# Optimization experiments

Hardware: AMD Instinct MI355X
Metric: run time of the kernel (lower is better)

## Reference

```python
import jax, jax.numpy as jnp
import numpy as np

N_A, N_B, C, M, E = 40000, 80000, 256, 4, 250000
NUM_HEADS = 4


def setup_inputs() -> dict:
    key = jax.random.key(0)
    ks = jax.random.split(key, 32)
    p = lambda k, shp: jax.random.normal(k, shp, dtype=jnp.float32) * 0.02
    src_ab = jax.random.randint(ks[0], (M, 1, E), 0, N_A, dtype=jnp.int32)
    dst_ab = jax.random.randint(ks[1], (M, 1, E), 0, N_B, dtype=jnp.int32)
    src_ba = jax.random.randint(ks[2], (M, 1, E), 0, N_B, dtype=jnp.int32)
    dst_ba = jax.random.randint(ks[3], (M, 1, E), 0, N_A, dtype=jnp.int32)
    mp_w = jax.random.uniform(ks[4], (M,), dtype=jnp.float32) + 0.1
    mp_w = mp_w / mp_w.sum()  # normalized metapath_counts buffer
    return {
        "x_a": jax.random.normal(ks[5], (N_A, C), jnp.float32),
        "x_b": jax.random.normal(ks[6], (N_B, C), jnp.float32),
        "edges_ab": jnp.concatenate([src_ab, dst_ab], axis=1),  # [M,2,E]
        "edges_ba": jnp.concatenate([src_ba, dst_ba], axis=1),  # [M,2,E]
        "wl1": p(ks[7], (M, C, C)), "wr1": p(ks[8], (M, C, C)), "b1": p(ks[9], (M, C)),
        "wl2": p(ks[10], (M, C, C)), "wr2": p(ks[11], (M, C, C)), "b2": p(ks[12], (M, C)),
        "outw": p(ks[13], (M, C, C)), "outb": p(ks[14], (M, C)),
        "mp_weights": mp_w,
        "in_proj_w": p(ks[15], (3 * C, C)), "in_proj_b": p(ks[16], (3 * C,)),
        "attn_out_w": p(ks[17], (C, C)), "attn_out_b": p(ks[18], (C,)),
        "mlp1_w": p(ks[19], (C, C)), "mlp1_b": p(ks[20], (C,)),
        "mlp2_w": p(ks[21], (C, 1)), "mlp2_b": p(ks[22], (1,)),
    }


def _sage(x_src, x_dst, src, dst, n_dst, wl, wr, b):
    # SAGEConv (mean aggr): lin_l(mean_{src->dst} x_src) + lin_r(x_dst) + b
    msg = jax.ops.segment_sum(x_src[src], dst, num_segments=n_dst)
    cnt = jax.ops.segment_sum(jnp.ones(src.shape, x_src.dtype), dst, num_segments=n_dst)
    mean = msg / jnp.maximum(cnt, 1.0)[:, None]
    return mean @ wl + x_dst @ wr + b


def _forward(x_a, x_b, edges_ab, edges_ba, wl1, wr1, b1, wl2, wr2, b2, outw, outb,
             mp_weights, in_proj_w, in_proj_b, attn_out_w, attn_out_b,
             mlp1_w, mlp1_b, mlp2_w, mlp2_b):
    embs = []
    for m in range(M):  # small fixed set of metapath GNNs (structurally distinct params)
        h_b = jax.nn.relu(_sage(x_a, x_b, edges_ab[m, 0], edges_ab[m, 1], N_B,
                                wl1[m], wr1[m], b1[m]))
        h_a = jax.nn.relu(_sage(h_b, x_a, edges_ba[m, 0], edges_ba[m, 1], N_A,
                                wl2[m], wr2[m], b2[m]))
        embs.append(h_a @ outw[m] + outb[m])  # out_proj on start node type
    x = jnp.stack(embs, axis=1) * mp_weights[None, :, None]  # [N_A, M, C]
    # MultiheadAttention (batch_first, self-attention over metapath axis)
    qkv = x @ in_proj_w.T + in_proj_b
    q, k, v = jnp.split(qkv, 3, axis=-1)
    d = C // NUM_HEADS
    q = q.reshape(N_A, M, NUM_HEADS, d)
    k = k.reshape(N_A, M, NUM_HEADS, d)
    v = v.reshape(N_A, M, NUM_HEADS, d)
    scores = jnp.einsum('nqhd,nkhd->nhqk', q, k) / jnp.sqrt(jnp.float32(d))
    attn = jax.nn.softmax(scores, axis=-1)
    o = jnp.einsum('nhqk,nkhd->nqhd', attn, v).reshape(N_A, M, C)
    o = o @ attn_out_w.T + attn_out_b
    pooled = o.mean(axis=1)  # [N_A, C]
    h = jax.nn.relu(pooled @ mlp1_w + mlp1_b)
    return (h @ mlp2_w + mlp2_b).squeeze(-1)  # [N_A]


def reference(x_a, x_b, edges_ab, edges_ba, wl1, wr1, b1, wl2, wr2, b2, outw, outb,
              mp_weights, in_proj_w, in_proj_b, attn_out_w, attn_out_b,
              mlp1_w, mlp1_b, mlp2_w, mlp2_b):
    return _forward(x_a, x_b, edges_ab, edges_ba, wl1, wr1, b1, wl2, wr2, b2,
                    outw, outb, mp_weights, in_proj_w, in_proj_b,
                    attn_out_w, attn_out_b, mlp1_w, mlp1_b, mlp2_w, mlp2_b)
```

## Files before the change

kernel.cpp:

```cpp
#include <hip/hip_runtime.h>
#include <hip/hip_bf16.h>
#include <hip/hip_fp16.h>


#define N_A 40000
#define N_B 80000
#define CDIM 256
#define MP 4
#define EDG 250000

using f16x8 = __attribute__((ext_vector_type(8))) _Float16;
using f32x4 = __attribute__((ext_vector_type(4))) float;

__device__ __forceinline__ float ldf(const float* p) { return *p; }
__device__ __forceinline__ float ldf(const __half* p) { return __half2float(*p); }
__device__ __forceinline__ void stf(float* p, float v) { *p = v; }
__device__ __forceinline__ void stf(__half* p, float v) { *p = __float2half(v); }

__device__ __forceinline__ float4 ld4(const __half* p) {
    __half2 a = *(const __half2*)p, b = *(const __half2*)(p + 2);
    float2 fa = __half22float2(a), fb = __half22float2(b);
    return make_float4(fa.x, fa.y, fb.x, fb.y);
}

template<typename AT, typename CT, typename ET, bool FUSE2, bool EXTRA,
         bool BIAS, bool RELU, bool OSCALE>
__global__ __launch_bounds__(256) void mgemm_k(
    const AT* __restrict__ A, int lda,
    const __half* __restrict__ A2,
    const __half* __restrict__ BT,
    const float* __restrict__ bias,
    const ET* __restrict__ extra, int lde,
    const float* __restrict__ osp, int osi,
    CT* __restrict__ C, int ldc, int K)
{
    __shared__ __align__(16) _Float16 As[64 * 40];
    __shared__ __align__(16) _Float16 Bs[128 * 40];
    const int tid = threadIdx.x;
    const int w = tid >> 6, lane = tid & 63;
    const int wm = w & 1, wn = w >> 1;
    const int lr = lane & 15, kb = lane >> 4;
    const long long row0 = (long long)blockIdx.y * 64;
    const int col0 = blockIdx.x * 128;
    f32x4 acc[2][4] = {};
    for (int k0 = 0; k0 < K; k0 += 32) {
        {
            int flat = tid * 8;
            int r = flat >> 5, c = flat & 31;
            int kk = k0 + c;
            if constexpr (FUSE2) {
                const __half* src = (kk < 256)
                    ? (const __half*)&A[(row0 + r) * lda + kk]
                    : &A2[(row0 + r) * 256 + (kk - 256)];
                *(f16x8*)&As[r * 40 + c] = *(const f16x8*)src;
            } else if constexpr (sizeof(AT) == 4) {
                const AT* src = &A[(row0 + r) * lda + kk];
                float4 v0 = *(const float4*)(src);
                float4 v1 = *(const float4*)(src + 4);
                _Float16 h[8] = {(_Float16)v0.x, (_Float16)v0.y, (_Float16)v0.z,
                                 (_Float16)v0.w, (_Float16)v1.x, (_Float16)v1.y,
                                 (_Float16)v1.z, (_Float16)v1.w};
                *(f16x8*)&As[r * 40 + c] = *(f16x8*)h;
            } else {
                *(f16x8*)&As[r * 40 + c] =
                    *(const f16x8*)&A[(row0 + r) * lda + kk];
            }
        }
        {
            #pragma unroll
            for (int q = 0; q < 2; ++q) {
                int cid = tid * 2 + q;
                int r = cid >> 2, cc = cid & 3;
                *(f16x8*)&Bs[r * 40 + cc * 8] =
                    *(const f16x8*)&BT[(long long)(col0 + r) * K + k0 + cc * 8];
            }
        }
        __syncthreads();
        f16x8 af[2], bf[4];
        #pragma unroll
        for (int i = 0; i < 2; ++i)
            af[i] = *(f16x8*)&As[(wm * 32 + i * 16 + lr) * 40 + kb * 8];
        #pragma unroll
        for (int j = 0; j < 4; ++j)
            bf[j] = *(f16x8*)&Bs[(wn * 64 + j * 16 + lr) * 40 + kb * 8];
        #pragma unroll
        for (int i = 0; i < 2; ++i)
            #pragma unroll
            for (int j = 0; j < 4; ++j)
                acc[i][j] = __builtin_amdgcn_mfma_f32_16x16x32_f16(
                    af[i], bf[j], acc[i][j], 0, 0, 0);
        __syncthreads();
    }
    float osc = 1.0f;
    if (OSCALE) osc = osp[osi];
    #pragma unroll
    for (int i = 0; i < 2; ++i) {
        #pragma unroll
        for (int j = 0; j < 4; ++j) {
            #pragma unroll
            for (int r = 0; r < 4; ++r) {
                long long rg = row0 + wm * 32 + i * 16 + (lane >> 4) * 4 + r;
                int cg = col0 + wn * 64 + j * 16 + (lane & 15);
                float v = acc[i][j][r];
                if (EXTRA) v += ldf(&extra[rg * lde + cg]);
                if (BIAS) v += bias[cg];
                if (RELU) v = fmaxf(v, 0.0f);
                if (OSCALE) v *= osc;
                stf(&C[rg * ldc + cg], v);
            }
        }
    }
}

__global__ void cvt8_k(const float* __restrict__ s, __half* __restrict__ d, int n8)
{
    int t = blockIdx.x * 256 + threadIdx.x;
    if (t >= n8) return;
    const float4 a = *(const float4*)&s[t * 8];
    const float4 b = *(const float4*)&s[t * 8 + 4];
    _Float16 h[8] = {(_Float16)a.x, (_Float16)a.y, (_Float16)a.z, (_Float16)a.w,
                     (_Float16)b.x, (_Float16)b.y, (_Float16)b.z, (_Float16)b.w};
    *(f16x8*)&d[t * 8] = *(f16x8*)h;
}
__global__ void cvt_flat_k(const float* __restrict__ s, __half* __restrict__ d, int n)
{
    int t = blockIdx.x * 256 + threadIdx.x;
    if (t < n) d[t] = __float2half(s[t]);
}
__global__ void cvt_tr_k(const float* __restrict__ s, __half* __restrict__ d, int ns)
{
    int t = blockIdx.x * 256 + threadIdx.x;
    if (t >= ns * 65536) return;
    int m = t >> 16, i = t & 65535;
    int r = i >> 8, c = i & 255;
    d[(m << 16) + (c << 8) + r] = __float2half(s[t]);
}
__global__ void cvt_bt2_k(const float* __restrict__ wr2,
                          const float* __restrict__ wl2, __half* __restrict__ d)
{
    int t = blockIdx.x * 256 + threadIdx.x;
    if (t >= 4 * 256 * 512) return;
    int m = t >> 17, i = t & 131071;
    int n = i >> 9, k = i & 511;
    float v = (k < 256) ? wr2[(m << 16) + (k << 8) + n]
                        : wl2[(m << 16) + ((k - 256) << 8) + n];
    d[t] = __float2half(v);
}
__global__ void wc_k(const float* __restrict__ aow, const float* __restrict__ m1w,
                     __half* __restrict__ wct)
{
    int t = blockIdx.x * 256 + threadIdx.x;
    if (t >= 65536) return;
    int n = t >> 8, k = t & 255;
    float s = 0.0f;
    for (int j = 0; j < 256; ++j)
        s = fmaf(aow[j * 256 + k], m1w[j * 256 + n], s);
    wct[t] = __float2half(s);
}
__global__ void bc_k(const float* __restrict__ aob, const float* __restrict__ m1w,
                     const float* __restrict__ m1b, float* __restrict__ bc)
{
    int n = threadIdx.x;
    float s = m1b[n];
    for (int j = 0; j < 256; ++j) s = fmaf(aob[j], m1w[j * 256 + n], s);
    bc[n] = s;
}

__global__ __launch_bounds__(256) void hist_k(
    const int* __restrict__ dst, int* __restrict__ cnt, int E)
{
    int e = blockIdx.x * 256 + threadIdx.x;
    if (e < E) atomicAdd(&cnt[dst[e]], 1);
}
__global__ __launch_bounds__(256) void scan_blk_k(
    const int* __restrict__ cnt, int* __restrict__ bsum, int n)
{
    __shared__ int s[256];
    int t = threadIdx.x, i = blockIdx.x * 256 + t;
    s[t] = (i < n) ? cnt[i] : 0;
    __syncthreads();
    for (int off = 128; off > 0; off >>= 1) {
        if (t < off) s[t] += s[t + off];
        __syncthreads();
    }
    if (t == 0) bsum[blockIdx.x] = s[0];
}
__global__ __launch_bounds__(512) void scan_top_k(
    const int* __restrict__ bsum, int* __restrict__ boff, int nb)
{
    __shared__ int s[512];
    int t = threadIdx.x;
    int v = (t < nb) ? bsum[t] : 0;
    s[t] = v;
    __syncthreads();
    for (int off = 1; off < 512; off <<= 1) {
        int u = (t >= off) ? s[t - off] : 0;
        __syncthreads();
        s[t] += u;
        __syncthreads();
    }
    if (t < nb) boff[t] = s[t] - v;
}
__global__ __launch_bounds__(256) void scan_fin_k(
    const int* __restrict__ cnt, const int* __restrict__ boff,
    int* __restrict__ start, int* __restrict__ cursor, int n)
{
    __shared__ int s[256];
    int t = threadIdx.x, i = blockIdx.x * 256 + t;
    int v = (i < n) ? cnt[i] : 0;
    s[t] = v;
    __syncthreads();
    for (int off = 1; off < 256; off <<= 1) {
        int u = (t >= off) ? s[t - off] : 0;
        __syncthreads();
        s[t] += u;
        __syncthreads();
    }
    if (i < n) {
        int ex = boff[blockIdx.x] + s[t] - v;
        start[i] = ex;
        cursor[i] = ex;
    }
}
__global__ __launch_bounds__(256) void fill_k(
    const int* __restrict__ src, const int* __restrict__ dst,
    int* __restrict__ cursor, int* __restrict__ eidx, int E)
{
    int e = blockIdx.x * 256 + threadIdx.x;
    if (e < E) {
        int p = atomicAdd(&cursor[dst[e]], 1);
        eidx[p] = src[e];
    }
}

__global__ __launch_bounds__(256) void gather_mean_k(
    const __half* __restrict__ feat, const int* __restrict__ start,
    const int* __restrict__ cnt, const int* __restrict__ eidx,
    __half* __restrict__ mean, int n)
{
    int t = blockIdx.x * 256 + threadIdx.x;
    int r = t >> 6, lane = t & 63;
    if (r >= n) return;
    const int s0 = start[r], deg = cnt[r];
    float4 acc = make_float4(0.f, 0.f, 0.f, 0.f);
    for (int i = 0; i < deg; ++i) {
        int s = eidx[s0 + i];
        float4 v = ld4(&feat[(long long)s * CDIM + lane * 4]);
        acc.x += v.x; acc.y += v.y; acc.z += v.z; acc.w += v.w;
    }
    const float inv = 1.0f / fmaxf((float)deg, 1.0f);
    __half hv[4] = {__float2half(acc.x * inv), __float2half(acc.y * inv),
                    __float2half(acc.z * inv), __float2half(acc.w * inv)};
    *(float2*)&mean[(long long)r * CDIM + lane * 4] = *(float2*)hv;
}

__global__ __launch_bounds__(256) void attn_pool_k(
    const __half* __restrict__ qkv, float* __restrict__ pooled, int nNodes)
{
    __shared__ float sh[4][3072];
    __shared__ float sW[4][16];
    const int tid = threadIdx.x;
    const int wid = tid >> 6, lane = tid & 63;
    const int node = blockIdx.x * 4 + wid;
    float* S = sh[wid];
    const __half* base = qkv + (long long)node * 3072;
    #pragma unroll
    for (int it = 0; it < 6; ++it) {
        int f = it * 64 + lane;
        f16x8 v = *(const f16x8*)&base[f * 8];
        #pragma unroll
        for (int e = 0; e < 8; ++e) S[f * 8 + e] = (float)v[e];
    }
    __syncthreads();
    const int h = lane >> 4, qm = (lane >> 2) & 3, km = lane & 3;
    const float* qrow = &S[qm * 768 + h * 64];
    const float* krow = &S[km * 768 + 256 + h * 64];
    float s = 0.0f;
    #pragma unroll
    for (int i = 0; i < 64; ++i) s = fmaf(qrow[i], krow[i], s);
    s *= 0.125f;
    float mx = fmaxf(s, __shfl_xor(s, 1));
    mx = fmaxf(mx, __shfl_xor(mx, 2));
    float e = __expf(s - mx);
    float sum = e + __shfl_xor(e, 1);
    sum += __shfl_xor(sum, 2);
    float a = e / sum;
    float tt = a + __shfl_xor(a, 4);
    tt += __shfl_xor(tt, 8);
    if (qm == 0) sW[wid][h * 4 + km] = 0.25f * tt;
    __syncthreads();
    #pragma unroll
    for (int j = 0; j < 4; ++j) {
        int c = j * 64 + lane;
        float p = 0.0f;
        #pragma unroll
        for (int kk = 0; kk < 4; ++kk)
            p = fmaf(sW[wid][j * 4 + kk], S[kk * 768 + 512 + c], p);
        pooled[(long long)node * 256 + c] = p;
    }
}

__global__ __launch_bounds__(256) void mlp2_k(
    const __half* __restrict__ h, const float* __restrict__ w,
    const float* __restrict__ b, float* __restrict__ out, int n)
{
    int t = blockIdx.x * 256 + threadIdx.x;
    int node = t >> 6, lane = t & 63;
    if (node >= n) return;
    const float4 hv = ld4(&h[(long long)node * CDIM + lane * 4]);
    const float4 wv = *(const float4*)&w[lane * 4];
    float s = hv.x * wv.x + hv.y * wv.y + hv.z * wv.z + hv.w * wv.w;
    #pragma unroll
    for (int off = 1; off < 64; off <<= 1) s += __shfl_xor(s, off);
    if (lane == 0) out[node] = s + b[0];
}

__global__ void diag_k(float* out, int n, float val)
{
    int t = blockIdx.x * 256 + threadIdx.x;
    if (t < n) out[t] = val;
}

extern "C" void kernel_launch(void* const* d_in, const int* in_sizes, int n_in,
                              void* d_out, int out_size, void* d_ws, size_t ws_size,
                              hipStream_t stream)
{
    const float* x_a  = (const float*)d_in[0];
    const float* x_b  = (const float*)d_in[1];
    const int*   e_ab = (const int*)d_in[2];
    const int*   e_ba = (const int*)d_in[3];
    const float* wl1  = (const float*)d_in[4];
    const float* wr1  = (const float*)d_in[5];
    const float* b1   = (const float*)d_in[6];
    const float* wl2  = (const float*)d_in[7];
    const float* wr2  = (const float*)d_in[8];
    const float* b2   = (const float*)d_in[9];
    const float* outw = (const float*)d_in[10];
    const float* outb = (const float*)d_in[11];
    const float* mpw  = (const float*)d_in[12];
    const float* ipw  = (const float*)d_in[13];
    const float* ipb  = (const float*)d_in[14];
    const float* aow  = (const float*)d_in[15];
    const float* aob  = (const float*)d_in[16];
    const float* m1w  = (const float*)d_in[17];
    const float* m1b  = (const float*)d_in[18];
    const float* m2w  = (const float*)d_in[19];
    const float* m2b  = (const float*)d_in[20];
    float* out = (float*)d_out;

    const size_t NEED = 40960000ull + 82240000ull + 40960000ull + 81920000ull
                      + 786432ull + 262144ull;
    if (ws_size < NEED || n_in < 21 || out_size != N_A) {
        float diag = (float)((ws_size / (1024ull * 1024ull)) * 100ull + (size_t)n_in);
        diag_k<<<(out_size + 255) / 256, 256, 0, stream>>>(out, out_size, diag);
        return;
    }

    char* base = (char*)d_ws;
    __half* XA16 = (__half*)(base);
    __half* XB16 = (__half*)(base + 20480000);
    __half* WH   = (__half*)(base + 61440000);
    char*   AREG = base + 65634304;
    char*   BREG = base + 106594304;
    __half* EMBS = (__half*)(base + 147554304);
    __half* WL1T  = WH;
    __half* WR1T  = WH + 262144;
    __half* BT2   = WH + 524288;
    __half* OUTWT = WH + 1048576;
    __half* IPW16 = WH + 1310720;
    __half* WCT   = WH + 1507328;
    float*  BC    = (float*)(WH + 1572864);
    __half* ZH     = (__half*)AREG;
    __half* HBH    = (__half*)AREG;
    __half* HA16   = (__half*)AREG;
    __half* QKVC16 = (__half*)AREG;
    __half* TMLP16 = (__half*)AREG;
    __half* MEANB16 = (__half*)BREG;
    __half* MEANA16 = (__half*)BREG;
    float*  POOL    = (float*)BREG;
    int* cntB   = (int*)(AREG + 20480000);
    int* startB = cntB + N_B;
    int* cursB  = cntB + 2 * N_B;
    int* eidxB  = cntB + 3 * N_B;
    int* bsumB  = eidxB + EDG;
    int* boffB  = bsumB + 512;
    int* cntA   = (int*)(BREG + 20480000);
    int* startA = cntA + N_A;
    int* cursA  = cntA + 2 * N_A;
    int* eidxA  = cntA + 3 * N_A;
    int* bsumA  = eidxA + EDG;
    int* boffA  = bsumA + 512;

    cvt8_k<<<5000, 256, 0, stream>>>(x_a, XA16, 1280000);
    cvt8_k<<<10000, 256, 0, stream>>>(x_b, XB16, 2560000);
    cvt_tr_k<<<1024, 256, 0, stream>>>(wl1, WL1T, 4);
    cvt_tr_k<<<1024, 256, 0, stream>>>(wr1, WR1T, 4);
    cvt_tr_k<<<1024, 256, 0, stream>>>(outw, OUTWT, 4);
    cvt_bt2_k<<<2048, 256, 0, stream>>>(wr2, wl2, BT2);
    cvt_flat_k<<<768, 256, 0, stream>>>(ipw, IPW16, 196608);
    wc_k<<<256, 256, 0, stream>>>(aow, m1w, WCT);
    bc_k<<<1, 256, 0, stream>>>(aob, m1w, m1b, BC);

    const int EB = (EDG + 255) / 256;
    const int NBB = (N_B + 255) / 256;
    const int NBA = (N_A + 255) / 256;

    for (int m = 0; m < MP; ++m) {
        const int* sab = e_ab + (size_t)m * 2 * EDG;
        const int* dab = sab + EDG;
        const int* sba = e_ba + (size_t)m * 2 * EDG;
        const int* dba = sba + EDG;

        mgemm_k<__half, __half, float, false, false, false, false, false>
            <<<dim3(2, N_A / 64), 256, 0, stream>>>(
            XA16, CDIM, nullptr, WL1T + m * 65536, nullptr, nullptr, 0,
            nullptr, 0, ZH, CDIM, CDIM);
        hipMemsetAsync(cntB, 0, (size_t)N_B * 4, stream);
        hist_k<<<EB, 256, 0, stream>>>(dab, cntB, EDG);
        scan_blk_k<<<NBB, 256, 0, stream>>>(cntB, bsumB, N_B);
        scan_top_k<<<1, 512, 0, stream>>>(bsumB, boffB, NBB);
        scan_fin_k<<<NBB, 256, 0, stream>>>(cntB, boffB, startB, cursB, N_B);
        fill_k<<<EB, 256, 0, stream>>>(sab, dab, cursB, eidxB, EDG);
        gather_mean_k<<<N_B / 4, 256, 0, stream>>>(
            ZH, startB, cntB, eidxB, MEANB16, N_B);
        mgemm_k<__half, __half, __half, false, true, true, true, false>
            <<<dim3(2, N_B / 64), 256, 0, stream>>>(
            XB16, CDIM, nullptr, WR1T + m * 65536, b1 + (size_t)m * CDIM,
            MEANB16, CDIM, nullptr, 0, HBH, CDIM, CDIM);
        hipMemsetAsync(cntA, 0, (size_t)N_A * 4, stream);
        hist_k<<<EB, 256, 0, stream>>>(dba, cntA, EDG);
        scan_blk_k<<<NBA, 256, 0, stream>>>(cntA, bsumA, N_A);
        scan_top_k<<<1, 512, 0, stream>>>(bsumA, boffA, NBA);
        scan_fin_k<<<NBA, 256, 0, stream>>>(cntA, boffA, startA, cursA, N_A);
        fill_k<<<EB, 256, 0, stream>>>(sba, dba, cursA, eidxA, EDG);
        gather_mean_k<<<N_A / 4, 256, 0, stream>>>(
            HBH, startA, cntA, eidxA, MEANA16, N_A);
        mgemm_k<__half, __half, float, true, false, true, true, false>
            <<<dim3(2, N_A / 64), 256, 0, stream>>>(
            XA16, CDIM, MEANA16, BT2 + m * 131072, b2 + (size_t)m * CDIM,
            nullptr, 0, nullptr, 0, HA16, CDIM, 512);
        mgemm_k<__half, __half, float, false, false, true, false, true>
            <<<dim3(2, N_A / 64), 256, 0, stream>>>(
            HA16, CDIM, nullptr, OUTWT + m * 65536, outb + (size_t)m * CDIM,
            nullptr, 0, mpw, m, EMBS + (size_t)m * CDIM, 1024, CDIM);
    }

    const int CH = 4000;
    for (int ch = 0; ch < N_A / CH; ++ch) {
        const int n0 = ch * CH;
        mgemm_k<__half, __half, float, false, false, true, false, false>
            <<<dim3(6, (CH * 4) / 64), 256, 0, stream>>>(
            EMBS + (size_t)n0 * 1024, CDIM, nullptr, IPW16, ipb, nullptr, 0,
            nullptr, 0, QKVC16, 768, CDIM);
        attn_pool_k<<<CH / 4, 256, 0, stream>>>(QKVC16, POOL + (size_t)n0 * 256, CH);
    }
    mgemm_k<float, __half, float, false, false, true, true, false>
        <<<dim3(2, N_A / 64), 256, 0, stream>>>(
        POOL, CDIM, nullptr, WCT, BC, nullptr, 0, nullptr, 0, TMLP16, CDIM, CDIM);
    mlp2_k<<<(N_A * 64) / 256, 256, 0, stream>>>(TMLP16, m2w, m2b, out, N_A);
}
```

Measured before the change: 1.530 ms.

## Batch CSR builds and weight prep into fewer launches, fp16 pooled output

```diff
diff --git a/kernel.cpp b/kernel.cpp
--- a/kernel.cpp
+++ b/kernel.cpp
@@ -122,75 +122,81 @@
                      (_Float16)b.x, (_Float16)b.y, (_Float16)b.z, (_Float16)b.w};
     *(f16x8*)&d[t * 8] = *(f16x8*)h;
 }
-__global__ void cvt_flat_k(const float* __restrict__ s, __half* __restrict__ d, int n)
-{
-    int t = blockIdx.x * 256 + threadIdx.x;
-    if (t < n) d[t] = __float2half(s[t]);
-}
-__global__ void cvt_tr_k(const float* __restrict__ s, __half* __restrict__ d, int ns)
-{
-    int t = blockIdx.x * 256 + threadIdx.x;
-    if (t >= ns * 65536) return;
-    int m = t >> 16, i = t & 65535;
-    int r = i >> 8, c = i & 255;
-    d[(m << 16) + (c << 8) + r] = __float2half(s[t]);
-}
-__global__ void cvt_bt2_k(const float* __restrict__ wr2,
-                          const float* __restrict__ wl2, __half* __restrict__ d)
-{
-    int t = blockIdx.x * 256 + threadIdx.x;
-    if (t >= 4 * 256 * 512) return;
-    int m = t >> 17, i = t & 131071;
-    int n = i >> 9, k = i & 511;
-    float v = (k < 256) ? wr2[(m << 16) + (k << 8) + n]
-                        : wl2[(m << 16) + ((k - 256) << 8) + n];
-    d[t] = __float2half(v);
-}
-__global__ void wc_k(const float* __restrict__ aow, const float* __restrict__ m1w,
-                     __half* __restrict__ wct)
-{
-    int t = blockIdx.x * 256 + threadIdx.x;
-    if (t >= 65536) return;
-    int n = t >> 8, k = t & 255;
-    float s = 0.0f;
-    for (int j = 0; j < 256; ++j)
-        s = fmaf(aow[j * 256 + k], m1w[j * 256 + n], s);
-    wct[t] = __float2half(s);
-}
-__global__ void bc_k(const float* __restrict__ aob, const float* __restrict__ m1w,
-                     const float* __restrict__ m1b, float* __restrict__ bc)
-{
-    int n = threadIdx.x;
-    float s = m1b[n];
-    for (int j = 0; j < 256; ++j) s = fmaf(aob[j], m1w[j * 256 + n], s);
-    bc[n] = s;
-}
-
-__global__ __launch_bounds__(256) void hist_k(
-    const int* __restrict__ dst, int* __restrict__ cnt, int E)
-{
-    int e = blockIdx.x * 256 + threadIdx.x;
-    if (e < E) atomicAdd(&cnt[dst[e]], 1);
-}
-__global__ __launch_bounds__(256) void scan_blk_k(
-    const int* __restrict__ cnt, int* __restrict__ bsum, int n)
+
+__global__ __launch_bounds__(256) void prep_k(
+    const float* __restrict__ wl1, const float* __restrict__ wr1,
+    const float* __restrict__ outw, const float* __restrict__ wr2,
+    const float* __restrict__ wl2, const float* __restrict__ ipw,
+    const float* __restrict__ aow, const float* __restrict__ m1w,
+    const float* __restrict__ aob, const float* __restrict__ m1b,
+    __half* __restrict__ WL1T, __half* __restrict__ WR1T,
+    __half* __restrict__ OUTWT, __half* __restrict__ BT2,
+    __half* __restrict__ IPW16, __half* __restrict__ WCT,
+    float* __restrict__ BC)
+{
+    const int sec = blockIdx.y;
+    const int t = blockIdx.x * 256 + threadIdx.x;
+    if (sec < 3) {
+        if (t >= 262144) return;
+        const float* s = (sec == 0) ? wl1 : (sec == 1) ? wr1 : outw;
+        __half* d = (sec == 0) ? WL1T : (sec == 1) ? WR1T : OUTWT;
+        int m = t >> 16, i = t & 65535, r = i >> 8, c = i & 255;
+        d[(m << 16) + (c << 8) + r] = __float2half(s[t]);
+    } else if (sec == 3) {
+        if (t >= 524288) return;
+        int m = t >> 17, i = t & 131071, n = i >> 9, k = i & 511;
+        float v = (k < 256) ? wr2[(m << 16) + (k << 8) + n]
+                            : wl2[(m << 16) + ((k - 256) << 8) + n];
+        BT2[t] = __float2half(v);
+    } else if (sec == 4) {
+        if (t >= 196608) return;
+        IPW16[t] = __float2half(ipw[t]);
+    } else if (sec == 5) {
+        if (t >= 65536) return;
+        int n = t >> 8, k = t & 255;
+        float s = 0.0f;
+        for (int j = 0; j < 256; ++j)
+            s = fmaf(aow[j * 256 + k], m1w[j * 256 + n], s);
+        WCT[t] = __float2half(s);
+    } else {
+        if (t >= 256) return;
+        float s = m1b[t];
+        for (int j = 0; j < 256; ++j) s = fmaf(aob[j], m1w[j * 256 + t], s);
+        BC[t] = s;
+    }
+}
+
+__global__ __launch_bounds__(256) void hist_all_k(
+    const int* __restrict__ e_ab, const int* __restrict__ e_ba,
+    int* __restrict__ cnt_all)
+{
+    const int l = blockIdx.y;
+    const int e = blockIdx.x * 256 + threadIdx.x;
+    if (e >= EDG) return;
+    const int m = l >> 1, dir = l & 1;
+    const int* dst = (dir ? e_ba : e_ab) + (size_t)m * 2 * EDG + EDG;
+    atomicAdd(&cnt_all[l * 80000 + dst[e]], 1);
+}
+__global__ __launch_bounds__(256) void scan_blk_all_k(
+    const int* __restrict__ cnt_all, int* __restrict__ bsum_all)
 {
     __shared__ int s[256];
-    int t = threadIdx.x, i = blockIdx.x * 256 + t;
-    s[t] = (i < n) ? cnt[i] : 0;
+    const int l = blockIdx.y, t = threadIdx.x;
+    const int i = blockIdx.x * 256 + t;
+    s[t] = (i < 80000) ? cnt_all[l * 80000 + i] : 0;
     __syncthreads();
     for (int off = 128; off > 0; off >>= 1) {
         if (t < off) s[t] += s[t + off];
         __syncthreads();
     }
-    if (t == 0) bsum[blockIdx.x] = s[0];
-}
-__global__ __launch_bounds__(512) void scan_top_k(
-    const int* __restrict__ bsum, int* __restrict__ boff, int nb)
+    if (t == 0) bsum_all[l * 313 + blockIdx.x] = s[0];
+}
+__global__ __launch_bounds__(512) void scan_top_all_k(
+    const int* __restrict__ bsum_all, int* __restrict__ boff_all)
 {
     __shared__ int s[512];
-    int t = threadIdx.x;
-    int v = (t < nb) ? bsum[t] : 0;
+    const int l = blockIdx.x, t = threadIdx.x;
+    int v = (t < 313) ? bsum_all[l * 313 + t] : 0;
     s[t] = v;
     __syncthreads();
     for (int off = 1; off < 512; off <<= 1) {
@@ -199,15 +205,16 @@
         s[t] += u;
         __syncthreads();
     }
-    if (t < nb) boff[t] = s[t] - v;
-}
-__global__ __launch_bounds__(256) void scan_fin_k(
-    const int* __restrict__ cnt, const int* __restrict__ boff,
-    int* __restrict__ start, int* __restrict__ cursor, int n)
+    if (t < 313) boff_all[l * 313 + t] = s[t] - v;
+}
+__global__ __launch_bounds__(256) void scan_fin_all_k(
+    const int* __restrict__ cnt_all, const int* __restrict__ boff_all,
+    int* __restrict__ start_all, int* __restrict__ cursor_all)
 {
     __shared__ int s[256];
-    int t = threadIdx.x, i = blockIdx.x * 256 + t;
-    int v = (i < n) ? cnt[i] : 0;
+    const int l = blockIdx.y, t = threadIdx.x;
+    const int i = blockIdx.x * 256 + t;
+    int v = (i < 80000) ? cnt_all[l * 80000 + i] : 0;
     s[t] = v;
     __syncthreads();
     for (int off = 1; off < 256; off <<= 1) {
@@ -216,21 +223,24 @@
         s[t] += u;
         __syncthreads();
     }
-    if (i < n) {
-        int ex = boff[blockIdx.x] + s[t] - v;
-        start[i] = ex;
-        cursor[i] = ex;
-    }
-}
-__global__ __launch_bounds__(256) void fill_k(
-    const int* __restrict__ src, const int* __restrict__ dst,
-    int* __restrict__ cursor, int* __restrict__ eidx, int E)
-{
-    int e = blockIdx.x * 256 + threadIdx.x;
-    if (e < E) {
-        int p = atomicAdd(&cursor[dst[e]], 1);
-        eidx[p] = src[e];
-    }
+    if (i < 80000) {
+        int ex = boff_all[l * 313 + blockIdx.x] + s[t] - v;
+        start_all[l * 80000 + i] = ex;
+        cursor_all[l * 80000 + i] = ex;
+    }
+}
+__global__ __launch_bounds__(256) void fill_all_k(
+    const int* __restrict__ e_ab, const int* __restrict__ e_ba,
+    int* __restrict__ cursor_all, int* __restrict__ eidx_all)
+{
+    const int l = blockIdx.y;
+    const int e = blockIdx.x * 256 + threadIdx.x;
+    if (e >= EDG) return;
+    const int m = l >> 1, dir = l & 1;
+    const int* src = (dir ? e_ba : e_ab) + (size_t)m * 2 * EDG;
+    const int* dst = src + EDG;
+    int p = atomicAdd(&cursor_all[l * 80000 + dst[e]], 1);
+    eidx_all[l * 250000 + p] = src[e];
 }
 
 __global__ __launch_bounds__(256) void gather_mean_k(
@@ -255,7 +265,7 @@
 }
 
 __global__ __launch_bounds__(256) void attn_pool_k(
-    const __half* __restrict__ qkv, float* __restrict__ pooled, int nNodes)
+    const __half* __restrict__ qkv, __half* __restrict__ pooled, int nNodes)
 {
     __shared__ float sh[4][3072];
     __shared__ float sW[4][16];
@@ -296,7 +306,7 @@
         #pragma unroll
         for (int kk = 0; kk < 4; ++kk)
             p = fmaf(sW[wid][j * 4 + kk], S[kk * 768 + 512 + c], p);
-        pooled[(long long)node * 256 + c] = p;
+        pooled[(long long)node * 256 + c] = __float2half(p);
     }
 }
 
@@ -363,6 +373,7 @@
     char*   AREG = base + 65634304;
     char*   BREG = base + 106594304;
     __half* EMBS = (__half*)(base + 147554304);
+    int*    CSR  = (int*)(base + 229474304);
     __half* WL1T  = WH;
     __half* WR1T  = WH + 262144;
     __half* BT2   = WH + 524288;
@@ -370,71 +381,52 @@
     __half* IPW16 = WH + 1310720;
     __half* WCT   = WH + 1507328;
     float*  BC    = (float*)(WH + 1572864);
-    __half* ZH     = (__half*)AREG;
-    __half* HBH    = (__half*)AREG;
-    __half* HA16   = (__half*)AREG;
-    __half* QKVC16 = (__half*)AREG;
-    __half* TMLP16 = (__half*)AREG;
+    int* cnt_all    = CSR;
+    int* start_all  = CSR + 640000;
+    int* cursor_all = CSR + 1280000;
+    int* eidx_all   = CSR + 1920000;
+    int* bsum_all   = CSR + 3920000;
+    int* boff_all   = CSR + 3922504;
+    __half* ZH      = (__half*)AREG;
+    __half* HBH     = (__half*)AREG;
     __half* MEANB16 = (__half*)BREG;
     __half* MEANA16 = (__half*)BREG;
-    float*  POOL    = (float*)BREG;
-    int* cntB   = (int*)(AREG + 20480000);
-    int* startB = cntB + N_B;
-    int* cursB  = cntB + 2 * N_B;
-    int* eidxB  = cntB + 3 * N_B;
-    int* bsumB  = eidxB + EDG;
-    int* boffB  = bsumB + 512;
-    int* cntA   = (int*)(BREG + 20480000);
-    int* startA = cntA + N_A;
-    int* cursA  = cntA + 2 * N_A;
-    int* eidxA  = cntA + 3 * N_A;
-    int* bsumA  = eidxA + EDG;
-    int* boffA  = bsumA + 512;
+    __half* HA16    = (__half*)(BREG + 20480000);
+    __half* QKV16   = (__half*)AREG;
+    __half* POOL16  = (__half*)(AREG + 61440000);
+    __half* TMLP16  = (__half*)AREG;
 
     cvt8_k<<<5000, 256, 0, stream>>>(x_a, XA16, 1280000);
     cvt8_k<<<10000, 256, 0, stream>>>(x_b, XB16, 2560000);
-    cvt_tr_k<<<1024, 256, 0, stream>>>(wl1, WL1T, 4);
-    cvt_tr_k<<<1024, 256, 0, stream>>>(wr1, WR1T, 4);
-    cvt_tr_k<<<1024, 256, 0, stream>>>(outw, OUTWT, 4);
-    cvt_bt2_k<<<2048, 256, 0, stream>>>(wr2, wl2, BT2);
-    cvt_flat_k<<<768, 256, 0, stream>>>(ipw, IPW16, 196608);
-    wc_k<<<256, 256, 0, stream>>>(aow, m1w, WCT);
-    bc_k<<<1, 256, 0, stream>>>(aob, m1w, m1b, BC);
+    prep_k<<<dim3(2048, 7), 256, 0, stream>>>(
+        wl1, wr1, outw, wr2, wl2, ipw, aow, m1w, aob, m1b,
+        WL1T, WR1T, OUTWT, BT2, IPW16, WCT, BC);
 
     const int EB = (EDG + 255) / 256;
-    const int NBB = (N_B + 255) / 256;
-    const int NBA = (N_A + 255) / 256;
+    hipMemsetAsync(cnt_all, 0, 640000 * 4, stream);
+    hist_all_k<<<dim3(EB, 8), 256, 0, stream>>>(e_ab, e_ba, cnt_all);
+    scan_blk_all_k<<<dim3(313, 8), 256, 0, stream>>>(cnt_all, bsum_all);
+    scan_top_all_k<<<8, 512, 0, stream>>>(bsum_all, boff_all);
+    scan_fin_all_k<<<dim3(313, 8), 256, 0, stream>>>(cnt_all, boff_all,
+                                                     start_all, cursor_all);
+    fill_all_k<<<dim3(EB, 8), 256, 0, stream>>>(e_ab, e_ba, cursor_all, eidx_all);
 
     for (int m = 0; m < MP; ++m) {
-        const int* sab = e_ab + (size_t)m * 2 * EDG;
-        const int* dab = sab + EDG;
-        const int* sba = e_ba + (size_t)m * 2 * EDG;
-        const int* dba = sba + EDG;
-
+        const int lB = 2 * m, lA = 2 * m + 1;
         mgemm_k<__half, __half, float, false, false, false, false, false>
             <<<dim3(2, N_A / 64), 256, 0, stream>>>(
             XA16, CDIM, nullptr, WL1T + m * 65536, nullptr, nullptr, 0,
             nullptr, 0, ZH, CDIM, CDIM);
-        hipMemsetAsync(cntB, 0, (size_t)N_B * 4, stream);
-        hist_k<<<EB, 256, 0, stream>>>(dab, cntB, EDG);
-        scan_blk_k<<<NBB, 256, 0, stream>>>(cntB, bsumB, N_B);
-        scan_top_k<<<1, 512, 0, stream>>>(bsumB, boffB, NBB);
-        scan_fin_k<<<NBB, 256, 0, stream>>>(cntB, boffB, startB, cursB, N_B);
-        fill_k<<<EB, 256, 0, stream>>>(sab, dab, cursB, eidxB, EDG);
         gather_mean_k<<<N_B / 4, 256, 0, stream>>>(
-            ZH, startB, cntB, eidxB, MEANB16, N_B);
+            ZH, start_all + lB * 80000, cnt_all + lB * 80000,
+            eidx_all + lB * 250000, MEANB16, N_B);
         mgemm_k<__half, __half, __half, false, true, true, true, false>
             <<<dim3(2, N_B / 64), 256, 0, stream>>>(
             XB16, CDIM, nullptr, WR1T + m * 65536, b1 + (size_t)m * CDIM,
             MEANB16, CDIM, nullptr, 0, HBH, CDIM, CDIM);
-        hipMemsetAsync(cntA, 0, (size_t)N_A * 4, stream);
-        hist_k<<<EB, 256, 0, stream>>>(dba, cntA, EDG);
-        scan_blk_k<<<NBA, 256, 0, stream>>>(cntA, bsumA, N_A);
-        scan_top_k<<<1, 512, 0, stream>>>(bsumA, boffA, NBA);
-        scan_fin_k<<<NBA, 256, 0, stream>>>(cntA, boffA, startA, cursA, N_A);
-        fill_k<<<EB, 256, 0, stream>>>(sba, dba, cursA, eidxA, EDG);
         gather_mean_k<<<N_A / 4, 256, 0, stream>>>(
-            HBH, startA, cntA, eidxA, MEANA16, N_A);
+            HBH, start_all + lA * 80000, cnt_all + lA * 80000,
+            eidx_all + lA * 250000, MEANA16, N_A);
         mgemm_k<__half, __half, float, true, false, true, true, false>
             <<<dim3(2, N_A / 64), 256, 0, stream>>>(
             XA16, CDIM, MEANA16, BT2 + m * 131072, b2 + (size_t)m * CDIM,
@@ -445,17 +437,19 @@
             nullptr, 0, mpw, m, EMBS + (size_t)m * CDIM, 1024, CDIM);
     }
 
-    const int CH = 4000;
+    const int CH = 10000;
     for (int ch = 0; ch < N_A / CH; ++ch) {
         const int n0 = ch * CH;
         mgemm_k<__half, __half, float, false, false, true, false, false>
             <<<dim3(6, (CH * 4) / 64), 256, 0, stream>>>(
             EMBS + (size_t)n0 * 1024, CDIM, nullptr, IPW16, ipb, nullptr, 0,
-            nullptr, 0, QKVC16, 768, CDIM);
-        attn_pool_k<<<CH / 4, 256, 0, stream>>>(QKVC16, POOL + (size_t)n0 * 256, CH);
-    }
-    mgemm_k<float, __half, float, false, false, true, true, false>
+            nullptr, 0, QKV16, 768, CDIM);
+        attn_pool_k<<<CH / 4, 256, 0, stream>>>(
+            QKV16, POOL16 + (size_t)n0 * 256, CH);
+    }
+    mgemm_k<__half, __half, float, false, false, true, true, false>
         <<<dim3(2, N_A / 64), 256, 0, stream>>>(
-        POOL, CDIM, nullptr, WCT, BC, nullptr, 0, nullptr, 0, TMLP16, CDIM, CDIM);
+        POOL16, CDIM, nullptr, WCT, BC, nullptr, 0, nullptr, 0,
+        TMLP16, CDIM, CDIM);
     mlp2_k<<<(N_A * 64) / 256, 256, 0, stream>>>(TMLP16, m2w, m2b, out, N_A);
 }
```

After: 1.372 ms. 10.3% less time.
